# Performance work log

Measured on AMD Instinct MI355X. Metric: run time of the kernel, lower is better.

## Reference

```python
import jax, jax.numpy as jnp
import numpy as np
from jax import lax


def _grey_opening_2d(x, size):
    """scipy.ndimage.grey_opening(x, size) per 2D map, applied over trailing (H, W).

    Grey opening = erosion (min filter) then dilation (max filter) with a
    size x size flat structuring element. scipy uses mode='reflect'
    (== np.pad 'symmetric') and, for even sizes, an asymmetric window:
    erosion covers offsets [-(size//2), size - size//2 - 1], dilation uses
    the mirrored offsets. x: [B, C, H, W].
    """
    lo = size // 2
    hi = size - size // 2 - 1
    window = (1, 1, size, size)
    ones = (1, 1, 1, 1)

    # Erosion: min filter, window offsets [-lo, hi]
    xe = jnp.pad(x, ((0, 0), (0, 0), (lo, hi), (lo, hi)), mode='symmetric')
    er = lax.reduce_window(xe, jnp.inf, lax.min, window, ones, 'VALID')

    # Dilation: max filter with mirrored structuring element -> offsets [-hi, lo]
    xd = jnp.pad(er, ((0, 0), (0, 0), (hi, lo), (hi, lo)), mode='symmetric')
    di = lax.reduce_window(xd, -jnp.inf, lax.max, window, ones, 'VALID')
    return di


def setup_inputs() -> dict:
    key = jax.random.key(0)
    labels = jax.random.uniform(key, (16, 8, 512, 512), dtype=jnp.float32)
    return {"labels": labels}


def reference(labels):
    radius = 2
    smooth = _grey_opening_2d(labels, radius)
    smooth = lax.stop_gradient(smooth)  # original detaches the opened target
    return jnp.mean((labels - smooth) ** 2)
```

## Files before the change

kernel.cpp:

```cpp
#include <hip/hip_runtime.h>


constexpr int W = 512;
constexpr int H = 512;
constexpr int RPW = 16;
constexpr int STRIPS = H / RPW;

__global__ __launch_bounds__(256) void open_loss(
    const float* __restrict__ x, float* __restrict__ out, float invN) {
  const int gtid = blockIdx.x * blockDim.x + threadIdx.x;
  const int wave = gtid >> 6;
  const int lane = threadIdx.x & 63;
  const int img = wave >> 5;
  const int strip = wave & (STRIPS - 1);

  const float* base =
      x + ((size_t)img * H + (size_t)strip * RPW) * W + (size_t)lane * 8;

  float v[8], cm[8], cm8;
  float pcm[8], pcm8;
  float xp[8], dmp[8];
  const int loff = (lane == 0) ? 0 : -1;
  const int roff = (lane == 63) ? 7 : 8;

  auto loadrow = [&](int drow) {
    const float* p = base + (ptrdiff_t)drow * W;
    float4 a = *reinterpret_cast<const float4*>(p);
    float4 b = *reinterpret_cast<const float4*>(p + 4);
    v[0] = a.x; v[1] = a.y; v[2] = a.z; v[3] = a.w;
    v[4] = b.x; v[5] = b.y; v[6] = b.z; v[7] = b.w;
    const float left = p[loff];
    const float right = p[roff];
    cm[0] = fminf(left, v[0]);
#pragma unroll
    for (int k = 1; k < 8; ++k) cm[k] = fminf(v[k - 1], v[k]);
    cm8 = fminf(v[7], right);
  };

  loadrow(strip ? -1 : 0);
#pragma unroll
  for (int k = 0; k < 8; ++k) pcm[k] = cm[k];
  pcm8 = cm8;

  loadrow(0);
  {
    float er[8];
#pragma unroll
    for (int k = 0; k < 8; ++k) er[k] = fminf(pcm[k], cm[k]);
    const float er8 = fminf(pcm8, cm8);
#pragma unroll
    for (int k = 0; k < 7; ++k) dmp[k] = fmaxf(er[k], er[k + 1]);
    dmp[7] = fmaxf(er[7], er8);
#pragma unroll
    for (int k = 0; k < 8; ++k) { xp[k] = v[k]; pcm[k] = cm[k]; }
    pcm8 = cm8;
  }

  float acc = 0.f;

  auto advance = [&](int drow_next) {
    loadrow(drow_next);
    float er[8], dmn[8];
#pragma unroll
    for (int k = 0; k < 8; ++k) er[k] = fminf(pcm[k], cm[k]);
    const float er8 = fminf(pcm8, cm8);
#pragma unroll
    for (int k = 0; k < 7; ++k) dmn[k] = fmaxf(er[k], er[k + 1]);
    dmn[7] = fmaxf(er[7], er8);
#pragma unroll
    for (int k = 0; k < 8; ++k) {
      const float d = xp[k] - fmaxf(dmp[k], dmn[k]);
      acc = fmaf(d, d, acc);
      xp[k] = v[k]; pcm[k] = cm[k]; dmp[k] = dmn[k];
    }
    pcm8 = cm8;
  };

#pragma unroll 5
  for (int r = 1; r <= RPW - 1; ++r) advance(r);

  if (strip != STRIPS - 1) {
    advance(RPW);
  } else {
#pragma unroll
    for (int k = 0; k < 8; ++k) {
      const float d = xp[k] - dmp[k];
      acc = fmaf(d, d, acc);
    }
  }

#pragma unroll
  for (int off = 32; off > 0; off >>= 1) acc += __shfl_down(acc, off);
  __shared__ float sh[4];
  const int wid = threadIdx.x >> 6;
  if (lane == 0) sh[wid] = acc;
  __syncthreads();
  if (threadIdx.x == 0) {
    atomicAdd(out, (sh[0] + sh[1] + sh[2] + sh[3]) * invN);
  }
}

extern "C" void kernel_launch(void* const* d_in, const int* in_sizes, int n_in,
                              void* d_out, int out_size, void* d_ws, size_t ws_size,
                              hipStream_t stream) {
  const float* x = (const float*)d_in[0];
  float* out = (float*)d_out;

  const long long n = in_sizes[0];
  const int nImg = (int)(n / ((long long)H * W));
  const int nWaves = nImg * STRIPS;
  const int nBlocks = nWaves / 4;

  const float invN = 1.0f / (float)n;

  hipMemsetAsync(out, 0, sizeof(float), stream);
  open_loss<<<nBlocks, 256, 0, stream>>>(x, out, invN);
}
```

Before: 193.8 us.

## Split each row across two waves with 4 columns per lane and shuffle halos

Each wave now covers half a row (256 columns, 4 per lane) instead of a full row, which doubles the number of waves. Neighbour columns are exchanged with wave shuffles instead of extra scalar global loads, and only the edge lane of each half loads the one out-of-half element. This aims to raise occupancy and memory-level parallelism and to cut redundant loads. In exchange it adds cross-lane shuffle latency on every row and reloads the vertical halo rows for twice as many waves.

Result: slower. 198.8 us (+2.6%).

```diff
diff --git a/kernel.cpp b/kernel.cpp
--- a/kernel.cpp
+++ b/kernel.cpp
@@ -11,79 +11,81 @@
   const int gtid = blockIdx.x * blockDim.x + threadIdx.x;
   const int wave = gtid >> 6;
   const int lane = threadIdx.x & 63;
-  const int img = wave >> 5;
-  const int strip = wave & (STRIPS - 1);
+  const int img = wave >> 6;
+  const int rem = wave & 63;
+  const int half = rem & 1;
+  const int strip = rem >> 1;
 
-  const float* base =
-      x + ((size_t)img * H + (size_t)strip * RPW) * W + (size_t)lane * 8;
+  const float* base = x + ((size_t)img * H + (size_t)strip * RPW) * W +
+                      (size_t)half * 256 + (size_t)lane * 4;
+  const int extLane = half ? 0 : 63;
+  const int extOff = half ? -1 : 4;
 
-  float v[8], cm[8], cm8;
-  float pcm[8], pcm8;
-  float xp[8], dmp[8];
-  const int loff = (lane == 0) ? 0 : -1;
-  const int roff = (lane == 63) ? 7 : 8;
+  float v[4];
+  float cm[5];
+  float pcm[5];
+  float xp[4], dmp[4];
+  float acc = 0.f;
 
   auto loadrow = [&](int drow) {
     const float* p = base + (ptrdiff_t)drow * W;
-    float4 a = *reinterpret_cast<const float4*>(p);
-    float4 b = *reinterpret_cast<const float4*>(p + 4);
+    const float4 a = *reinterpret_cast<const float4*>(p);
     v[0] = a.x; v[1] = a.y; v[2] = a.z; v[3] = a.w;
-    v[4] = b.x; v[5] = b.y; v[6] = b.z; v[7] = b.w;
-    const float left = p[loff];
-    const float right = p[roff];
-    cm[0] = fminf(left, v[0]);
-#pragma unroll
-    for (int k = 1; k < 8; ++k) cm[k] = fminf(v[k - 1], v[k]);
-    cm8 = fminf(v[7], right);
+    float ext = 0.f;
+    if (lane == extLane) ext = p[extOff];
+    float vleft = __shfl_up(v[3], 1);
+    float vn0 = __shfl_down(v[0], 1);
+    if (lane == 0) vleft = half ? ext : v[0];
+    if (lane == 63) vn0 = half ? v[3] : ext;
+    cm[0] = fminf(vleft, v[0]);
+    cm[1] = fminf(v[0], v[1]);
+    cm[2] = fminf(v[1], v[2]);
+    cm[3] = fminf(v[2], v[3]);
+    cm[4] = fminf(v[3], vn0);
   };
 
   loadrow(strip ? -1 : 0);
 #pragma unroll
-  for (int k = 0; k < 8; ++k) pcm[k] = cm[k];
-  pcm8 = cm8;
+  for (int k = 0; k < 5; ++k) pcm[k] = cm[k];
 
   loadrow(0);
   {
-    float er[8];
+    float er[5];
 #pragma unroll
-    for (int k = 0; k < 8; ++k) er[k] = fminf(pcm[k], cm[k]);
-    const float er8 = fminf(pcm8, cm8);
+    for (int k = 0; k < 5; ++k) er[k] = fminf(pcm[k], cm[k]);
 #pragma unroll
-    for (int k = 0; k < 7; ++k) dmp[k] = fmaxf(er[k], er[k + 1]);
-    dmp[7] = fmaxf(er[7], er8);
+    for (int k = 0; k < 4; ++k) dmp[k] = fmaxf(er[k], er[k + 1]);
 #pragma unroll
-    for (int k = 0; k < 8; ++k) { xp[k] = v[k]; pcm[k] = cm[k]; }
-    pcm8 = cm8;
+    for (int k = 0; k < 4; ++k) xp[k] = v[k];
+#pragma unroll
+    for (int k = 0; k < 5; ++k) pcm[k] = cm[k];
   }
-
-  float acc = 0.f;
 
   auto advance = [&](int drow_next) {
     loadrow(drow_next);
-    float er[8], dmn[8];
+    float er[5], dm[4];
 #pragma unroll
-    for (int k = 0; k < 8; ++k) er[k] = fminf(pcm[k], cm[k]);
-    const float er8 = fminf(pcm8, cm8);
+    for (int k = 0; k < 5; ++k) er[k] = fminf(pcm[k], cm[k]);
 #pragma unroll
-    for (int k = 0; k < 7; ++k) dmn[k] = fmaxf(er[k], er[k + 1]);
-    dmn[7] = fmaxf(er[7], er8);
+    for (int k = 0; k < 4; ++k) dm[k] = fmaxf(er[k], er[k + 1]);
 #pragma unroll
-    for (int k = 0; k < 8; ++k) {
-      const float d = xp[k] - fmaxf(dmp[k], dmn[k]);
+    for (int k = 0; k < 4; ++k) {
+      const float d = xp[k] - fmaxf(dmp[k], dm[k]);
       acc = fmaf(d, d, acc);
-      xp[k] = v[k]; pcm[k] = cm[k]; dmp[k] = dmn[k];
+      xp[k] = v[k]; dmp[k] = dm[k];
     }
-    pcm8 = cm8;
+#pragma unroll
+    for (int k = 0; k < 5; ++k) pcm[k] = cm[k];
   };
 
-#pragma unroll 5
-  for (int r = 1; r <= RPW - 1; ++r) advance(r);
+#pragma unroll
+  for (int r = 1; r < RPW; ++r) advance(r);
 
   if (strip != STRIPS - 1) {
     advance(RPW);
   } else {
 #pragma unroll
-    for (int k = 0; k < 8; ++k) {
+    for (int k = 0; k < 4; ++k) {
       const float d = xp[k] - dmp[k];
       acc = fmaf(d, d, acc);
     }
@@ -108,7 +110,7 @@
 
   const long long n = in_sizes[0];
   const int nImg = (int)(n / ((long long)H * W));
-  const int nWaves = nImg * STRIPS;
+  const int nWaves = nImg * STRIPS * 2;
   const int nBlocks = nWaves / 4;
 
   const float invN = 1.0f / (float)n;
```
